# Kernel tuning notes

Hardware: AMD Instinct MI355X
Metric: run time of the kernel (lower is better)

Reference implementation:

```python
import jax, jax.numpy as jnp
import numpy as np

B, S, DIM, H = 8, 2048, 128, 8
HD = DIM // H  # 16
SCALE = 1.0 / np.sqrt(256.0).astype(np.float32)  # faithful: original divides by sqrt(256)=16


def setup_inputs() -> dict:
    key = jax.random.key(0)
    ks = jax.random.split(key, 8)
    w_std = 1.0 / np.sqrt(DIM).astype(np.float32)
    return {
        "q": jax.random.normal(ks[0], (B, S, DIM), jnp.float32),
        "k": jax.random.normal(ks[1], (B, S, DIM), jnp.float32),
        "v": jax.random.normal(ks[2], (B, S, DIM), jnp.float32),
        "Wq": jax.random.normal(ks[3], (DIM, DIM), jnp.float32) * w_std,
        "bq": jnp.zeros((DIM,), jnp.float32),
        "Wk": jax.random.normal(ks[4], (DIM, DIM), jnp.float32) * w_std,
        "bk": jnp.zeros((DIM,), jnp.float32),
        "Wv": jax.random.normal(ks[5], (DIM, DIM), jnp.float32) * w_std,
        "bv": jnp.zeros((DIM,), jnp.float32),
        "Wo": jax.random.normal(ks[6], (DIM, DIM), jnp.float32) * w_std,
        "bo": jnp.zeros((DIM,), jnp.float32),
    }


def reference(q, k, v, Wq, bq, Wk, bk, Wv, bv, Wo, bo):
    # QKV projections
    Q = q @ Wq + bq  # [B,S,DIM]
    K = k @ Wk + bk
    V = v @ Wv + bv
    # split heads: [B,H,S,HD]
    Q = Q.reshape(B, S, H, HD).transpose(0, 2, 1, 3)
    K = K.reshape(B, S, H, HD).transpose(0, 2, 1, 3)
    V = V.reshape(B, S, H, HD).transpose(0, 2, 1, 3)
    # scaled dot-product attention (note non-standard scale 1/16)
    scores = jnp.einsum("bhqd,bhkd->bhqk", Q, K) * SCALE
    attn = jax.nn.softmax(scores, axis=-1)
    out = jnp.einsum("bhqk,bhkd->bhqd", attn, V)
    out = out.transpose(0, 2, 1, 3).reshape(B, S, DIM)
    return out @ Wo + bo
```

## Files before the change

### kernel.cpp

```cpp
#include <hip/hip_runtime.h>

typedef __attribute__((ext_vector_type(8))) short short8;
typedef __attribute__((ext_vector_type(16))) float f32x16;
typedef unsigned int uint;
typedef unsigned short ushort;

#define NS 2048
#define C1F 0.0901684400555602f

__device__ __forceinline__ ushort f2bf(float f) {
  uint u = __builtin_bit_cast(uint, f);
  u += 0x7fffu + ((u >> 16) & 1u);
  return (ushort)(u >> 16);
}
__device__ __forceinline__ uint cvt_pk_bf16(float lo, float hi_) {
  uint r;
  asm("v_cvt_pk_bf16_f32 %0, %1, %2" : "=v"(r) : "v"(lo), "v"(hi_));
  return r;
}
__device__ __forceinline__ float fast_exp2(float x) {
#if __has_builtin(__builtin_amdgcn_exp2f)
  return __builtin_amdgcn_exp2f(x);
#else
  return exp2f(x);
#endif
}
__device__ __forceinline__ void plswap(uint& a, uint& b) {
#if __has_builtin(__builtin_amdgcn_permlane32_swap)
  auto r = __builtin_amdgcn_permlane32_swap(a, b, false, false);
  a = r[0];
  b = r[1];
#else
  const int hi = (threadIdx.x & 63) >> 5;
  uint av = (uint)__shfl_xor((int)a, 32, 64);
  uint bv = (uint)__shfl_xor((int)b, 32, 64);
  uint na = hi ? bv : a;
  uint nb = hi ? b : av;
  a = na;
  b = nb;
#endif
}

__global__ __launch_bounds__(256) void qkv_mfma(
    const float* __restrict__ qin, const float* __restrict__ kin, const float* __restrict__ vin,
    const float* __restrict__ Wq, const float* __restrict__ bq,
    const float* __restrict__ Wk, const float* __restrict__ bk,
    const float* __restrict__ Wv, const float* __restrict__ bv,
    ushort* __restrict__ Qbf, ushort* __restrict__ Kbf, ushort* __restrict__ Vt) {
  __shared__ ushort Wt[128 * 136];
  __shared__ ushort Al[128 * 136];
  const int tid = threadIdx.x;
  const int p = blockIdx.y;
  const float* A = (p == 0) ? qin : (p == 1) ? kin : vin;
  const float* W = (p == 0) ? Wq : (p == 1) ? Wk : Wv;
  const float* bias = (p == 0) ? bq : (p == 1) ? bk : bv;
  const float wscale = (p == 0) ? C1F : 1.0f;
  const int rbase = blockIdx.x * 128;
  {
    const int n = tid & 127, kg = tid >> 7;
#pragma unroll
    for (int k8 = 0; k8 < 8; ++k8) {
      int k0 = k8 * 16 + kg * 8;
      float w[8];
#pragma unroll
      for (int j = 0; j < 8; ++j) w[j] = W[(k0 + j) * 128 + n] * wscale;
      uint4 pk;
      pk.x = cvt_pk_bf16(w[0], w[1]);
      pk.y = cvt_pk_bf16(w[2], w[3]);
      pk.z = cvt_pk_bf16(w[4], w[5]);
      pk.w = cvt_pk_bf16(w[6], w[7]);
      *reinterpret_cast<uint4*>(&Wt[n * 136 + k0]) = pk;
    }
  }
#pragma unroll
  for (int it = 0; it < 16; ++it) {
    int fl = it * 256 + tid;
    int r = fl >> 5, c4 = (fl & 31) << 2;
    float4 a = *reinterpret_cast<const float4*>(A + (size_t)(rbase + r) * 128 + c4);
    uint2 pk;
    pk.x = cvt_pk_bf16(a.x, a.y);
    pk.y = cvt_pk_bf16(a.z, a.w);
    *reinterpret_cast<uint2*>(&Al[r * 136 + c4]) = pk;
  }
  __syncthreads();
  const int lane = tid & 63, wid = tid >> 6;
  const int l31 = lane & 31, hi = lane >> 5;
  f32x16 acc[4];
#pragma unroll
  for (int nt = 0; nt < 4; ++nt)
#pragma unroll
    for (int i = 0; i < 16; ++i) acc[nt][i] = 0.f;
  const ushort* arow = &Al[(wid * 32 + l31) * 136 + hi * 8];
#pragma unroll
  for (int kk = 0; kk < 8; ++kk) {
    const short8 af = *reinterpret_cast<const short8*>(arow + kk * 16);
#pragma unroll
    for (int nt = 0; nt < 4; ++nt) {
      const short8 bf = *reinterpret_cast<const short8*>(&Wt[(nt * 32 + l31) * 136 + kk * 16 + hi * 8]);
      acc[nt] = __builtin_amdgcn_mfma_f32_32x32x16_bf16(af, bf, acc[nt], 0, 0, 0);
    }
  }
  const int bI = rbase >> 11;
  if (p < 2) {
    ushort* outp = (p == 0) ? Qbf : Kbf;
#pragma unroll
    for (int nt = 0; nt < 4; ++nt) {
      int c = nt * 32 + l31;
      int h = c >> 4, d = c & 15;
      float bb = bias[c] * wscale;
#pragma unroll
      for (int r = 0; r < 16; ++r) {
        int s = rbase + wid * 32 + ((r & 3) + ((r >> 2) << 3) + (hi << 2));
        int sl = s & 2047;
        outp[((size_t)((bI << 3) + h) * 2048 + sl) * 16 + d] = f2bf(acc[nt][r] + bb);
      }
    }
  } else {
    __syncthreads();
    ushort* CL = Wt;
#pragma unroll
    for (int nt = 0; nt < 4; ++nt) {
      int c = nt * 32 + l31;
      float bb = bias[c];
#pragma unroll
      for (int g = 0; g < 4; ++g) {
        uint2 pk;
        pk.x = cvt_pk_bf16(acc[nt][g * 4 + 0] + bb, acc[nt][g * 4 + 1] + bb);
        pk.y = cvt_pk_bf16(acc[nt][g * 4 + 2] + bb, acc[nt][g * 4 + 3] + bb);
        int sl0 = wid * 32 + g * 8 + (hi << 2);
        *reinterpret_cast<uint2*>(&CL[c * 136 + sl0]) = pk;
      }
    }
    __syncthreads();
    const int slb = rbase & 2047;
#pragma unroll
    for (int it = 0; it < 8; ++it) {
      int fl = it * 256 + tid;
      int c = fl >> 4, s8 = (fl & 15) * 8;
      short8 val = *reinterpret_cast<const short8*>(&CL[c * 136 + s8]);
      int h = c >> 4, d = c & 15;
      *reinterpret_cast<short8*>(&Vt[((size_t)((bI << 3) + h) * 16 + d) * 2048 + slb + s8]) = val;
    }
  }
}

__global__ __launch_bounds__(256) void attn_kernel(
    const ushort* __restrict__ Qbf, const ushort* __restrict__ Kbf,
    const ushort* __restrict__ Vt, ushort* __restrict__ aout) {
  __shared__ ushort Kl[256 * 24];
  __shared__ ushort Vl[17 * 264];
  const int tid = threadIdx.x;
  const int lane = tid & 63, wv = tid >> 6;
  const int l31 = lane & 31, hi = lane >> 5;
  const int qt = blockIdx.x, bh = blockIdx.y;
  for (int e = tid; e < 264; e += 256) Vl[16 * 264 + e] = 0x3F80;
  const int q0 = qt * 128 + wv * 32;
  const short8 qf = *reinterpret_cast<const short8*>(
      Qbf + ((size_t)bh * NS + q0 + l31) * 16 + hi * 8);
  f32x16 oac0, oac1, zc;
#pragma unroll
  for (int i = 0; i < 16; ++i) { oac0[i] = 0.f; oac1[i] = 0.f; zc[i] = 0.f; }
  const int vrow = (l31 < 17) ? l31 : 16;
  const ushort* vbase = &Vl[vrow * 264 + hi * 8];
  const ushort* kbl = &Kl[l31 * 24 + hi * 8];
  for (int t = 0; t < 8; ++t) {
    const int kbase = t * 256;
#pragma unroll
    for (int it = 0; it < 2; ++it) {
      int idx = it * 256 + tid;
      int key = idx >> 1, hh = idx & 1;
      *reinterpret_cast<short8*>(&Kl[key * 24 + hh * 8]) =
          *reinterpret_cast<const short8*>(Kbf + ((size_t)bh * NS + kbase + key) * 16 + hh * 8);
    }
#pragma unroll
    for (int it = 0; it < 2; ++it) {
      int idx = it * 256 + tid;
      int d = idx >> 5, c8 = (idx & 31) * 8;
      *reinterpret_cast<short8*>(&Vl[d * 264 + c8]) =
          *reinterpret_cast<const short8*>(Vt + ((size_t)bh * 16 + d) * NS + kbase + c8);
    }
    __syncthreads();
#pragma unroll
    for (int kt = 0; kt < 8; ++kt) {
      const short8 kf = *reinterpret_cast<const short8*>(kbl + kt * 768);
      f32x16 sc = __builtin_amdgcn_mfma_f32_32x32x16_bf16(kf, qf, zc, 0, 0, 0);
      float pr[16];
#pragma unroll
      for (int r = 0; r < 16; ++r) pr[r] = fast_exp2(sc[r]);
      {
        uint u0 = cvt_pk_bf16(pr[0], pr[1]);
        uint u1 = cvt_pk_bf16(pr[2], pr[3]);
        uint u2 = cvt_pk_bf16(pr[4], pr[5]);
        uint u3 = cvt_pk_bf16(pr[6], pr[7]);
        plswap(u0, u2);
        plswap(u1, u3);
        union { uint u[4]; short8 s8; } pf;
        pf.u[0] = u0; pf.u[1] = u1; pf.u[2] = u2; pf.u[3] = u3;
        const short8 vf = *reinterpret_cast<const short8*>(vbase + kt * 32);
        oac0 = __builtin_amdgcn_mfma_f32_32x32x16_bf16(pf.s8, vf, oac0, 0, 0, 0);
      }
      {
        uint u0 = cvt_pk_bf16(pr[8], pr[9]);
        uint u1 = cvt_pk_bf16(pr[10], pr[11]);
        uint u2 = cvt_pk_bf16(pr[12], pr[13]);
        uint u3 = cvt_pk_bf16(pr[14], pr[15]);
        plswap(u0, u2);
        plswap(u1, u3);
        union { uint u[4]; short8 s8; } pf;
        pf.u[0] = u0; pf.u[1] = u1; pf.u[2] = u2; pf.u[3] = u3;
        const short8 vf = *reinterpret_cast<const short8*>(vbase + kt * 32 + 16);
        oac1 = __builtin_amdgcn_mfma_f32_32x32x16_bf16(pf.s8, vf, oac1, 0, 0, 0);
      }
    }
    __syncthreads();
  }
  const int b = bh >> 3, h = bh & 7;
  const int d = l31;
#pragma unroll
  for (int r = 0; r < 16; ++r) {
    float ov = oac0[r] + oac1[r];
    float ls = __shfl(ov, 16 + (hi << 5), 64);
    if (d < 16) {
      int qrow = q0 + ((r & 3) + ((r >> 2) << 3) + (hi << 2));
      aout[((size_t)(b * NS + qrow)) * 128 + h * 16 + d] = f2bf(ov / ls);
    }
  }
}

__global__ __launch_bounds__(256) void out_mfma(
    const ushort* __restrict__ Ain, const float* __restrict__ Wo,
    const float* __restrict__ bo, float* __restrict__ out) {
  __shared__ ushort Wt[128 * 136];
  __shared__ ushort Al[64 * 136];
  const int tid = threadIdx.x;
  const int rbase = blockIdx.x * 64;
  {
    const int n = tid & 127, kg = tid >> 7;
#pragma unroll
    for (int k8 = 0; k8 < 8; ++k8) {
      int k0 = k8 * 16 + kg * 8;
      float w[8];
#pragma unroll
      for (int j = 0; j < 8; ++j) w[j] = Wo[(k0 + j) * 128 + n];
      uint4 pk;
      pk.x = cvt_pk_bf16(w[0], w[1]);
      pk.y = cvt_pk_bf16(w[2], w[3]);
      pk.z = cvt_pk_bf16(w[4], w[5]);
      pk.w = cvt_pk_bf16(w[6], w[7]);
      *reinterpret_cast<uint4*>(&Wt[n * 136 + k0]) = pk;
    }
  }
#pragma unroll
  for (int it = 0; it < 4; ++it) {
    int fl = it * 256 + tid;
    int r = fl >> 4, c8 = (fl & 15) * 8;
    *reinterpret_cast<short8*>(&Al[r * 136 + c8]) =
        *reinterpret_cast<const short8*>(Ain + (size_t)(rbase + r) * 128 + c8);
  }
  __syncthreads();
  const int lane = tid & 63, wid = tid >> 6;
  const int l31 = lane & 31, hi = lane >> 5;
  const int rh = wid >> 1, ch = wid & 1;
  f32x16 acc[2];
#pragma unroll
  for (int i = 0; i < 2; ++i)
#pragma unroll
    for (int j = 0; j < 16; ++j) acc[i][j] = 0.f;
  const ushort* arow = &Al[(rh * 32 + l31) * 136 + hi * 8];
#pragma unroll
  for (int kk = 0; kk < 8; ++kk) {
    const short8 af = *reinterpret_cast<const short8*>(arow + kk * 16);
#pragma unroll
    for (int i = 0; i < 2; ++i) {
      int nt = ch * 2 + i;
      const short8 bf = *reinterpret_cast<const short8*>(&Wt[(nt * 32 + l31) * 136 + kk * 16 + hi * 8]);
      acc[i] = __builtin_amdgcn_mfma_f32_32x32x16_bf16(af, bf, acc[i], 0, 0, 0);
    }
  }
#pragma unroll
  for (int i = 0; i < 2; ++i) {
    int c = (ch * 2 + i) * 32 + l31;
    float bb = bo[c];
#pragma unroll
    for (int r = 0; r < 16; ++r) {
      int s = rbase + rh * 32 + ((r & 3) + ((r >> 2) << 3) + (hi << 2));
      out[(size_t)s * 128 + c] = acc[i][r] + bb;
    }
  }
}

extern "C" void kernel_launch(void* const* d_in, const int* in_sizes, int n_in,
                              void* d_out, int out_size, void* d_ws, size_t ws_size,
                              hipStream_t stream) {
  const float* q  = (const float*)d_in[0];
  const float* k  = (const float*)d_in[1];
  const float* v  = (const float*)d_in[2];
  const float* Wq = (const float*)d_in[3];
  const float* bq = (const float*)d_in[4];
  const float* Wk = (const float*)d_in[5];
  const float* bk = (const float*)d_in[6];
  const float* Wv = (const float*)d_in[7];
  const float* bv = (const float*)d_in[8];
  const float* Wo = (const float*)d_in[9];
  const float* bo = (const float*)d_in[10];
  float* out = (float*)d_out;

  ushort* Qbf = (ushort*)d_out;
  ushort* Kbf = Qbf + 2097152;
  ushort* Vt  = (ushort*)d_ws;
  ushort* aout = Vt + 2097152;

  hipLaunchKernelGGL(qkv_mfma, dim3(128, 3), dim3(256), 0, stream,
                     q, k, v, Wq, bq, Wk, bk, Wv, bv, Qbf, Kbf, Vt);
  hipLaunchKernelGGL(attn_kernel, dim3(16, 64), dim3(256), 0, stream, Qbf, Kbf, Vt, aout);
  hipLaunchKernelGGL(out_mfma, dim3(256), dim3(256), 0, stream, aout, Wo, bo, out);
}
```

Baseline: 69.24 us.

## Switch pipeline to fp16, polynomial exp2, and double-buffer K/V tiles

Converts all intermediates and MFMAs from bf16 to fp16. In attention, the exp2 per score is replaced by packed-fp16 polynomial evaluation: a degree-4 polynomial in x/4, then squared twice. The Q weight scale is divided by 4 to match. K/V tile loads are double-buffered in shared memory with register prefetch, so global loads overlap compute and one barrier per tile is dropped. This risks fp16 overflow and polynomial accuracy loss for large scores, and the softmax still has no running max.

```diff
diff --git a/kernel.cpp b/kernel.cpp
--- a/kernel.cpp
+++ b/kernel.cpp
@@ -2,28 +2,22 @@
 
 typedef __attribute__((ext_vector_type(8))) short short8;
 typedef __attribute__((ext_vector_type(16))) float f32x16;
+typedef _Float16 h2 __attribute__((ext_vector_type(2)));
+typedef _Float16 h8 __attribute__((ext_vector_type(8)));
 typedef unsigned int uint;
 typedef unsigned short ushort;
 
 #define NS 2048
-#define C1F 0.0901684400555602f
-
-__device__ __forceinline__ ushort f2bf(float f) {
-  uint u = __builtin_bit_cast(uint, f);
-  u += 0x7fffu + ((u >> 16) & 1u);
-  return (ushort)(u >> 16);
-}
-__device__ __forceinline__ uint cvt_pk_bf16(float lo, float hi_) {
+#define C1F4 0.022542110013890054f
+
+__device__ __forceinline__ ushort f2h(float f) {
+  _Float16 h = (_Float16)f;
+  return __builtin_bit_cast(ushort, h);
+}
+__device__ __forceinline__ uint pkrtz_u(float a, float b) {
   uint r;
-  asm("v_cvt_pk_bf16_f32 %0, %1, %2" : "=v"(r) : "v"(lo), "v"(hi_));
+  asm("v_cvt_pkrtz_f16_f32 %0, %1, %2" : "=v"(r) : "v"(a), "v"(b));
   return r;
-}
-__device__ __forceinline__ float fast_exp2(float x) {
-#if __has_builtin(__builtin_amdgcn_exp2f)
-  return __builtin_amdgcn_exp2f(x);
-#else
-  return exp2f(x);
-#endif
 }
 __device__ __forceinline__ void plswap(uint& a, uint& b) {
 #if __has_builtin(__builtin_amdgcn_permlane32_swap)
@@ -46,15 +40,15 @@
     const float* __restrict__ Wq, const float* __restrict__ bq,
     const float* __restrict__ Wk, const float* __restrict__ bk,
     const float* __restrict__ Wv, const float* __restrict__ bv,
-    ushort* __restrict__ Qbf, ushort* __restrict__ Kbf, ushort* __restrict__ Vt) {
-  __shared__ ushort Wt[128 * 136];
-  __shared__ ushort Al[128 * 136];
+    ushort* __restrict__ Qh, ushort* __restrict__ Kh, ushort* __restrict__ Vt) {
+  __shared__ __align__(16) ushort Wt[128 * 136];
+  __shared__ __align__(16) ushort Al[128 * 136];
   const int tid = threadIdx.x;
   const int p = blockIdx.y;
   const float* A = (p == 0) ? qin : (p == 1) ? kin : vin;
   const float* W = (p == 0) ? Wq : (p == 1) ? Wk : Wv;
   const float* bias = (p == 0) ? bq : (p == 1) ? bk : bv;
-  const float wscale = (p == 0) ? C1F : 1.0f;
+  const float wscale = (p == 0) ? C1F4 : 1.0f;
   const int rbase = blockIdx.x * 128;
   {
     const int n = tid & 127, kg = tid >> 7;
@@ -65,10 +59,10 @@
 #pragma unroll
       for (int j = 0; j < 8; ++j) w[j] = W[(k0 + j) * 128 + n] * wscale;
       uint4 pk;
-      pk.x = cvt_pk_bf16(w[0], w[1]);
-      pk.y = cvt_pk_bf16(w[2], w[3]);
-      pk.z = cvt_pk_bf16(w[4], w[5]);
-      pk.w = cvt_pk_bf16(w[6], w[7]);
+      pk.x = pkrtz_u(w[0], w[1]);
+      pk.y = pkrtz_u(w[2], w[3]);
+      pk.z = pkrtz_u(w[4], w[5]);
+      pk.w = pkrtz_u(w[6], w[7]);
       *reinterpret_cast<uint4*>(&Wt[n * 136 + k0]) = pk;
     }
   }
@@ -78,8 +72,8 @@
     int r = fl >> 5, c4 = (fl & 31) << 2;
     float4 a = *reinterpret_cast<const float4*>(A + (size_t)(rbase + r) * 128 + c4);
     uint2 pk;
-    pk.x = cvt_pk_bf16(a.x, a.y);
-    pk.y = cvt_pk_bf16(a.z, a.w);
+    pk.x = pkrtz_u(a.x, a.y);
+    pk.y = pkrtz_u(a.z, a.w);
     *reinterpret_cast<uint2*>(&Al[r * 136 + c4]) = pk;
   }
   __syncthreads();
@@ -93,16 +87,16 @@
   const ushort* arow = &Al[(wid * 32 + l31) * 136 + hi * 8];
 #pragma unroll
   for (int kk = 0; kk < 8; ++kk) {
-    const short8 af = *reinterpret_cast<const short8*>(arow + kk * 16);
+    const h8 af = *reinterpret_cast<const h8*>(arow + kk * 16);
 #pragma unroll
     for (int nt = 0; nt < 4; ++nt) {
-      const short8 bf = *reinterpret_cast<const short8*>(&Wt[(nt * 32 + l31) * 136 + kk * 16 + hi * 8]);
-      acc[nt] = __builtin_amdgcn_mfma_f32_32x32x16_bf16(af, bf, acc[nt], 0, 0, 0);
+      const h8 bf = *reinterpret_cast<const h8*>(&Wt[(nt * 32 + l31) * 136 + kk * 16 + hi * 8]);
+      acc[nt] = __builtin_amdgcn_mfma_f32_32x32x16_f16(af, bf, acc[nt], 0, 0, 0);
     }
   }
   const int bI = rbase >> 11;
   if (p < 2) {
-    ushort* outp = (p == 0) ? Qbf : Kbf;
+    ushort* outp = (p == 0) ? Qh : Kh;
 #pragma unroll
     for (int nt = 0; nt < 4; ++nt) {
       int c = nt * 32 + l31;
@@ -112,7 +106,7 @@
       for (int r = 0; r < 16; ++r) {
         int s = rbase + wid * 32 + ((r & 3) + ((r >> 2) << 3) + (hi << 2));
         int sl = s & 2047;
-        outp[((size_t)((bI << 3) + h) * 2048 + sl) * 16 + d] = f2bf(acc[nt][r] + bb);
+        outp[((size_t)((bI << 3) + h) * 2048 + sl) * 16 + d] = f2h(acc[nt][r] + bb);
       }
     }
   } else {
@@ -125,8 +119,8 @@
 #pragma unroll
       for (int g = 0; g < 4; ++g) {
         uint2 pk;
-        pk.x = cvt_pk_bf16(acc[nt][g * 4 + 0] + bb, acc[nt][g * 4 + 1] + bb);
-        pk.y = cvt_pk_bf16(acc[nt][g * 4 + 2] + bb, acc[nt][g * 4 + 3] + bb);
+        pk.x = pkrtz_u(acc[nt][g * 4 + 0] + bb, acc[nt][g * 4 + 1] + bb);
+        pk.y = pkrtz_u(acc[nt][g * 4 + 2] + bb, acc[nt][g * 4 + 3] + bb);
         int sl0 = wid * 32 + g * 8 + (hi << 2);
         *reinterpret_cast<uint2*>(&CL[c * 136 + sl0]) = pk;
       }
@@ -145,75 +139,100 @@
 }
 
 __global__ __launch_bounds__(256) void attn_kernel(
-    const ushort* __restrict__ Qbf, const ushort* __restrict__ Kbf,
-    const ushort* __restrict__ Vt, ushort* __restrict__ aout) {
-  __shared__ ushort Kl[256 * 24];
-  __shared__ ushort Vl[17 * 264];
+    const ushort* __restrict__ Qh, const ushort* __restrict__ Kh,
+    const ushort* __restrict__ Vtg, ushort* __restrict__ aout) {
+  __shared__ __align__(16) ushort Kl[2][256 * 24];
+  __shared__ __align__(16) ushort Vl[2][17 * 264];
   const int tid = threadIdx.x;
   const int lane = tid & 63, wv = tid >> 6;
   const int l31 = lane & 31, hi = lane >> 5;
   const int qt = blockIdx.x, bh = blockIdx.y;
-  for (int e = tid; e < 264; e += 256) Vl[16 * 264 + e] = 0x3F80;
+  for (int e = tid; e < 264; e += 256) {
+    Vl[0][16 * 264 + e] = 0x3C00;
+    Vl[1][16 * 264 + e] = 0x3C00;
+  }
   const int q0 = qt * 128 + wv * 32;
-  const short8 qf = *reinterpret_cast<const short8*>(
-      Qbf + ((size_t)bh * NS + q0 + l31) * 16 + hi * 8);
+  const h8 qf = *reinterpret_cast<const h8*>(Qh + ((size_t)bh * NS + q0 + l31) * 16 + hi * 8);
   f32x16 oac0, oac1, zc;
 #pragma unroll
   for (int i = 0; i < 16; ++i) { oac0[i] = 0.f; oac1[i] = 0.f; zc[i] = 0.f; }
   const int vrow = (l31 < 17) ? l31 : 16;
-  const ushort* vbase = &Vl[vrow * 264 + hi * 8];
-  const ushort* kbl = &Kl[l31 * 24 + hi * 8];
+  const ushort* Kg = Kh + (size_t)bh * NS * 16;
+  const ushort* Vg = Vtg + (size_t)bh * 16 * NS;
+  const int key0 = tid >> 1, hh = tid & 1, vd = tid >> 5, vc = (tid & 31) * 8;
+  const h2 c4 = {(_Float16)0.00961813f, (_Float16)0.00961813f};
+  const h2 c3 = {(_Float16)0.05644170f, (_Float16)0.05644170f};
+  const h2 c2 = {(_Float16)0.24022650f, (_Float16)0.24022650f};
+  const h2 c1 = {(_Float16)0.69301530f, (_Float16)0.69301530f};
+  const h2 c0 = {(_Float16)1.0f, (_Float16)1.0f};
+
+  short8 rk0, rk1, rv0, rv1;
+#define LOADT(T)                                                              \
+  {                                                                           \
+    int kb = (T) * 256;                                                       \
+    rk0 = *reinterpret_cast<const short8*>(Kg + (size_t)(kb + key0) * 16 + hh * 8);       \
+    rk1 = *reinterpret_cast<const short8*>(Kg + (size_t)(kb + 128 + key0) * 16 + hh * 8); \
+    rv0 = *reinterpret_cast<const short8*>(Vg + (size_t)vd * NS + kb + vc);               \
+    rv1 = *reinterpret_cast<const short8*>(Vg + (size_t)(8 + vd) * NS + kb + vc);         \
+  }
+#define WRITET(Bf)                                                            \
+  {                                                                           \
+    *reinterpret_cast<short8*>(&Kl[Bf][key0 * 24 + hh * 8]) = rk0;            \
+    *reinterpret_cast<short8*>(&Kl[Bf][(128 + key0) * 24 + hh * 8]) = rk1;    \
+    *reinterpret_cast<short8*>(&Vl[Bf][vd * 264 + vc]) = rv0;                 \
+    *reinterpret_cast<short8*>(&Vl[Bf][(8 + vd) * 264 + vc]) = rv1;           \
+  }
+
+  LOADT(0);
+  WRITET(0);
+  __syncthreads();
   for (int t = 0; t < 8; ++t) {
-    const int kbase = t * 256;
-#pragma unroll
-    for (int it = 0; it < 2; ++it) {
-      int idx = it * 256 + tid;
-      int key = idx >> 1, hh = idx & 1;
-      *reinterpret_cast<short8*>(&Kl[key * 24 + hh * 8]) =
-          *reinterpret_cast<const short8*>(Kbf + ((size_t)bh * NS + kbase + key) * 16 + hh * 8);
-    }
-#pragma unroll
-    for (int it = 0; it < 2; ++it) {
-      int idx = it * 256 + tid;
-      int d = idx >> 5, c8 = (idx & 31) * 8;
-      *reinterpret_cast<short8*>(&Vl[d * 264 + c8]) =
-          *reinterpret_cast<const short8*>(Vt + ((size_t)bh * 16 + d) * NS + kbase + c8);
-    }
-    __syncthreads();
+    const int cur = t & 1;
+    if (t < 7) LOADT(t + 1);
+    const ushort* kp = &Kl[cur][l31 * 24 + hi * 8];
+    const ushort* vp = &Vl[cur][vrow * 264 + hi * 8];
 #pragma unroll
     for (int kt = 0; kt < 8; ++kt) {
-      const short8 kf = *reinterpret_cast<const short8*>(kbl + kt * 768);
-      f32x16 sc = __builtin_amdgcn_mfma_f32_32x32x16_bf16(kf, qf, zc, 0, 0, 0);
-      float pr[16];
-#pragma unroll
-      for (int r = 0; r < 16; ++r) pr[r] = fast_exp2(sc[r]);
+      const h8 kf = *reinterpret_cast<const h8*>(kp + kt * 768);
+      f32x16 sc = __builtin_amdgcn_mfma_f32_32x32x16_f16(kf, qf, zc, 0, 0, 0);
+      uint ue[8];
+#pragma unroll
+      for (int j = 0; j < 8; ++j) {
+        h2 y = __builtin_bit_cast(h2, pkrtz_u(sc[2 * j], sc[2 * j + 1]));
+        h2 pp = __builtin_elementwise_fma(y, c4, c3);
+        pp = __builtin_elementwise_fma(pp, y, c2);
+        pp = __builtin_elementwise_fma(pp, y, c1);
+        pp = __builtin_elementwise_fma(pp, y, c0);
+        pp = pp * pp;
+        pp = pp * pp;
+        ue[j] = __builtin_bit_cast(uint, pp);
+      }
       {
-        uint u0 = cvt_pk_bf16(pr[0], pr[1]);
-        uint u1 = cvt_pk_bf16(pr[2], pr[3]);
-        uint u2 = cvt_pk_bf16(pr[4], pr[5]);
-        uint u3 = cvt_pk_bf16(pr[6], pr[7]);
+        uint u0 = ue[0], u1 = ue[1], u2 = ue[2], u3 = ue[3];
         plswap(u0, u2);
         plswap(u1, u3);
-        union { uint u[4]; short8 s8; } pf;
+        union { uint u[4]; h8 h; } pf;
         pf.u[0] = u0; pf.u[1] = u1; pf.u[2] = u2; pf.u[3] = u3;
-        const short8 vf = *reinterpret_cast<const short8*>(vbase + kt * 32);
-        oac0 = __builtin_amdgcn_mfma_f32_32x32x16_bf16(pf.s8, vf, oac0, 0, 0, 0);
+        const h8 vf = *reinterpret_cast<const h8*>(vp + kt * 32);
+        oac0 = __builtin_amdgcn_mfma_f32_32x32x16_f16(pf.h, vf, oac0, 0, 0, 0);
       }
       {
-        uint u0 = cvt_pk_bf16(pr[8], pr[9]);
-        uint u1 = cvt_pk_bf16(pr[10], pr[11]);
-        uint u2 = cvt_pk_bf16(pr[12], pr[13]);
-        uint u3 = cvt_pk_bf16(pr[14], pr[15]);
+        uint u0 = ue[4], u1 = ue[5], u2 = ue[6], u3 = ue[7];
         plswap(u0, u2);
         plswap(u1, u3);
-        union { uint u[4]; short8 s8; } pf;
+        union { uint u[4]; h8 h; } pf;
         pf.u[0] = u0; pf.u[1] = u1; pf.u[2] = u2; pf.u[3] = u3;
-        const short8 vf = *reinterpret_cast<const short8*>(vbase + kt * 32 + 16);
-        oac1 = __builtin_amdgcn_mfma_f32_32x32x16_bf16(pf.s8, vf, oac1, 0, 0, 0);
-      }
-    }
-    __syncthreads();
-  }
+        const h8 vf = *reinterpret_cast<const h8*>(vp + kt * 32 + 16);
+        oac1 = __builtin_amdgcn_mfma_f32_32x32x16_f16(pf.h, vf, oac1, 0, 0, 0);
+      }
+    }
+    if (t < 7) {
+      WRITET(cur ^ 1);
+      __syncthreads();
+    }
+  }
+#undef LOADT
+#undef WRITET
   const int b = bh >> 3, h = bh & 7;
   const int d = l31;
 #pragma unroll
@@ -222,7 +241,7 @@
     float ls = __shfl(ov, 16 + (hi << 5), 64);
     if (d < 16) {
       int qrow = q0 + ((r & 3) + ((r >> 2) << 3) + (hi << 2));
-      aout[((size_t)(b * NS + qrow)) * 128 + h * 16 + d] = f2bf(ov / ls);
+      aout[((size_t)(b * NS + qrow)) * 128 + h * 16 + d] = f2h(ov / ls);
     }
   }
 }
@@ -230,8 +249,8 @@
 __global__ __launch_bounds__(256) void out_mfma(
     const ushort* __restrict__ Ain, const float* __restrict__ Wo,
     const float* __restrict__ bo, float* __restrict__ out) {
-  __shared__ ushort Wt[128 * 136];
-  __shared__ ushort Al[64 * 136];
+  __shared__ __align__(16) ushort Wt[128 * 136];
+  __shared__ __align__(16) ushort Al[64 * 136];
   const int tid = threadIdx.x;
   const int rbase = blockIdx.x * 64;
   {
@@ -243,10 +262,10 @@
 #pragma unroll
       for (int j = 0; j < 8; ++j) w[j] = Wo[(k0 + j) * 128 + n];
       uint4 pk;
-      pk.x = cvt_pk_bf16(w[0], w[1]);
-      pk.y = cvt_pk_bf16(w[2], w[3]);
-      pk.z = cvt_pk_bf16(w[4], w[5]);
-      pk.w = cvt_pk_bf16(w[6], w[7]);
+      pk.x = pkrtz_u(w[0], w[1]);
+      pk.y = pkrtz_u(w[2], w[3]);
+      pk.z = pkrtz_u(w[4], w[5]);
+      pk.w = pkrtz_u(w[6], w[7]);
       *reinterpret_cast<uint4*>(&Wt[n * 136 + k0]) = pk;
     }
   }
@@ -269,12 +288,12 @@
   const ushort* arow = &Al[(rh * 32 + l31) * 136 + hi * 8];
 #pragma unroll
   for (int kk = 0; kk < 8; ++kk) {
-    const short8 af = *reinterpret_cast<const short8*>(arow + kk * 16);
+    const h8 af = *reinterpret_cast<const h8*>(arow + kk * 16);
 #pragma unroll
     for (int i = 0; i < 2; ++i) {
       int nt = ch * 2 + i;
-      const short8 bf = *reinterpret_cast<const short8*>(&Wt[(nt * 32 + l31) * 136 + kk * 16 + hi * 8]);
-      acc[i] = __builtin_amdgcn_mfma_f32_32x32x16_bf16(af, bf, acc[i], 0, 0, 0);
+      const h8 bf = *reinterpret_cast<const h8*>(&Wt[(nt * 32 + l31) * 136 + kk * 16 + hi * 8]);
+      acc[i] = __builtin_amdgcn_mfma_f32_32x32x16_f16(af, bf, acc[i], 0, 0, 0);
     }
   }
 #pragma unroll
@@ -305,13 +324,13 @@
   const float* bo = (const float*)d_in[10];
   float* out = (float*)d_out;
 
-  ushort* Qbf = (ushort*)d_out;
-  ushort* Kbf = Qbf + 2097152;
-  ushort* Vt  = (ushort*)d_ws;
+  ushort* Qh = (ushort*)d_out;
+  ushort* Kh = Qh + 2097152;
+  ushort* Vt = (ushort*)d_ws;
   ushort* aout = Vt + 2097152;
 
   hipLaunchKernelGGL(qkv_mfma, dim3(128, 3), dim3(256), 0, stream,
-                     q, k, v, Wq, bq, Wk, bk, Wv, bv, Qbf, Kbf, Vt);
-  hipLaunchKernelGGL(attn_kernel, dim3(16, 64), dim3(256), 0, stream, Qbf, Kbf, Vt, aout);
+                     q, k, v, Wq, bq, Wk, bk, Wv, bv, Qh, Kh, Vt);
+  hipLaunchKernelGGL(attn_kernel, dim3(16, 64), dim3(256), 0, stream, Qh, Kh, Vt, aout);
   hipLaunchKernelGGL(out_mfma, dim3(256), dim3(256), 0, stream, aout, Wo, bo, out);
 }
```

Result: slower. 75.33 us (+8.8%).
